# Optimization experiments

Measured on AMD Instinct MI355X. Metric: run time of the kernel, lower is better.

## Reference

```python
import jax, jax.numpy as jnp
import numpy as np

S = 10        # spiking_segment_count
TEMP = 50.0

def setup_inputs() -> dict:
    key = jax.random.key(0)
    ks = jax.random.split(key, 6)
    bs, din, dout = 2048, 1024, 1024
    x = jax.random.normal(ks[0], (bs, din), dtype=jnp.float32)
    t = jax.random.uniform(ks[1], (bs,), dtype=jnp.float32)  # in [0,1) subset of [-1,1]
    scale = 1.0 / np.sqrt(din)
    param_W = jax.random.normal(ks[2], (din, dout * S * 3), dtype=jnp.float32) * scale
    param_b = jax.random.normal(ks[3], (dout * S * 3,), dtype=jnp.float32) * 0.01
    norm_W = jax.random.normal(ks[4], (din, dout), dtype=jnp.float32) * scale
    norm_b = jax.random.normal(ks[5], (dout,), dtype=jnp.float32) * 0.01
    return {"x": x, "t": t, "param_W": param_W, "param_b": param_b,
            "norm_W": norm_W, "norm_b": norm_b}

def reference(x, t, param_W, param_b, norm_W, norm_b):
    bs = x.shape[0]
    dout = norm_W.shape[1]
    # param GEMM -> (bs, S, dout, 3)
    params = (x @ param_W + param_b).reshape(bs, S, dout, 3)
    weights = jax.nn.softmax(params[..., 0], axis=1)                 # (bs, S, dout)
    keypoints = jnp.concatenate(
        [jnp.zeros_like(weights[:, :1]), jnp.cumsum(weights, axis=1)], axis=1
    ) * 2.0 - 1.0                                                    # (bs, S+1, dout)
    slopes = jnp.tanh(params[..., 1])
    intercepts = params[..., 2]
    tt = t.reshape(-1, 1, 1)                                         # (bs, 1, 1)
    starts = keypoints[:, :S]
    ends = keypoints[:, 1:]
    residual = slopes * tt + intercepts                              # (bs, S, dout)
    validity = ((tt >= starts) & (tt < ends)) | ((tt == 1.0) & (ends == 1.0))
    vf = validity.astype(x.dtype)
    left_margin = jnp.sum((tt - starts) * vf, axis=1)                # (bs, dout)
    right_margin = jnp.sum((ends - tt) * vf, axis=1)
    lw = jax.nn.sigmoid(-TEMP * left_margin)
    rw = jax.nn.sigmoid(-TEMP * right_margin)
    lv = jnp.concatenate([vf[:, :1], vf[:, :-1]], axis=1)
    rv = jnp.concatenate([vf[:, 1:], vf[:, -1:]], axis=1)
    sw = -(lw + rw - 1.0)
    result = (lw * jnp.sum(residual * lv, axis=1)
              + sw * jnp.sum(residual * vf, axis=1)
              + rw * jnp.sum(residual * rv, axis=1))
    # norm == 'constant': subtract segment-wise integral, add norm_net(x)
    integral = jnp.sum(0.5 * slopes * (ends * ends - starts * starts)
                       + intercepts * weights, axis=1) * 0.5
    norm_target = x @ norm_W + norm_b
    return result - integral + norm_target
```

## Files before the change

kernel.cpp:

```cpp
#include <hip/hip_runtime.h>
#include <cstdint>
#include <cstddef>

#define BS    2048
#define DIN   1024
#define DOUT  1024
#define SSEG  10
#define NPAR  30720
#define NPK   20480
#define NCOL2 21504
#define NLG   10240
#define TAU   5e-5f
#define WL_CAP 1048576u

#define NB_SPLIT 2048
#define NB_NORM  1024
#define NB_TRW   2560

#define GEMM_BLKS 992

typedef _Float16 half_t;
typedef __attribute__((ext_vector_type(8))) _Float16 half8;
typedef __attribute__((ext_vector_type(4))) _Float16 half4;
typedef __attribute__((ext_vector_type(2))) _Float16 half2v;
typedef __attribute__((ext_vector_type(4))) float   floatx4;

__device__ __forceinline__ void gload16(const void* g, void* l) {
  __builtin_amdgcn_global_load_lds(
      (const __attribute__((address_space(1))) void*)g,
      (__attribute__((address_space(3))) void*)l, 16, 0, 0);
}

__global__ void k_zero(unsigned* c) { if (threadIdx.x == 0) *c = 0; }

__global__ __launch_bounds__(256) void k_prep(const float* __restrict__ x,
                                              half_t* __restrict__ xh,
                                              half_t* __restrict__ xl,
                                              const float* __restrict__ nW,
                                              const float* __restrict__ pW,
                                              half_t* __restrict__ wsm,
                                              half_t* __restrict__ wh,
                                              half_t* __restrict__ wlo,
                                              float* __restrict__ wlt,
                                              unsigned* __restrict__ cnt) {
  __shared__ float tile[32][384];
  int bid = blockIdx.x;
  int tid = threadIdx.x;

  if (bid < NB_SPLIT) {
    if (bid == 0 && tid == 0) *cnt = 0;
    int i = bid * 256 + tid;
    floatx4 v = ((const floatx4*)x)[i];
    half4 h, l;
    #pragma unroll
    for (int c = 0; c < 4; c++) { h[c] = (half_t)v[c]; l[c] = (half_t)(v[c] - (float)h[c]); }
    ((half4*)xh)[i] = h;
    ((half4*)xl)[i] = l;
    return;
  }

  if (bid < NB_SPLIT + NB_NORM) {
    int b2 = bid - NB_SPLIT;
    int col0 = (b2 & 31) * 32;
    int k0   = (b2 >> 5) * 32;
    int tx = tid & 31;
    int ty = tid >> 5;
    float* t33 = &tile[0][0];
    #pragma unroll
    for (int r = ty; r < 32; r += 8)
      t33[r * 33 + tx] = nW[(size_t)(k0 + r) * DOUT + col0 + tx];
    __syncthreads();
    #pragma unroll
    for (int r = ty; r < 32; r += 8)
      wsm[(size_t)(col0 + r + NPK) * DIN + k0 + tx] = (half_t)t33[tx * 33 + r];
    return;
  }

  int b3 = bid - NB_SPLIT - NB_NORM;
  int bx = b3 % 80;
  int k0 = (b3 / 80) * 32;
  int s  = bx >> 3;
  int d0 = (bx & 7) * 128;

  const float* sb = pW + (size_t)k0 * NPAR + bx * 384;
  for (int i = tid; i < 32 * 96; i += 256) {
    int r = i / 96, q = i - r * 96;
    ((floatx4*)&tile[r][0])[q] = ((const floatx4*)(sb + (size_t)r * NPAR))[q];
  }
  __syncthreads();

  for (int ci = tid; ci < 3072; ci += 256) {
    if (ci < 1024) {
      int rl = ci >> 2, kc = ci & 3;
      int jj = rl >> 1, cbit = rl & 1;
      int col = 3 * jj + 1 + cbit;
      half8 v;
      #pragma unroll
      for (int m = 0; m < 8; m++) v[m] = (half_t)tile[kc * 8 + m][col];
      *(half8*)(wsm + (size_t)(s * 2048 + 2 * (d0 + jj) + cbit) * DIN + k0 + kc * 8) = v;
    } else if (ci < 1536) {
      int u = ci - 1024;
      int jj = u >> 2, kc = u & 3;
      half8 v;
      #pragma unroll
      for (int m = 0; m < 8; m++) v[m] = (half_t)(tile[kc * 8 + m][3 * jj] * 32.0f);
      *(half8*)(wh + (size_t)(s * 1024 + d0 + jj) * DIN + k0 + kc * 8) = v;
    } else if (ci < 2048) {
      int u = ci - 1536;
      int jj = u >> 2, kc = u & 3;
      half8 v;
      #pragma unroll
      for (int m = 0; m < 8; m++) {
        float raw = tile[kc * 8 + m][3 * jj] * 32.0f;
        half_t h = (half_t)raw;
        v[m] = (half_t)(raw - (float)h);
      }
      *(half8*)(wlo + (size_t)(s * 1024 + d0 + jj) * DIN + k0 + kc * 8) = v;
    } else {
      int u = ci - 2048;
      int jj = u >> 3, kc = u & 7;
      floatx4 v;
      #pragma unroll
      for (int m = 0; m < 4; m++) v[m] = tile[kc * 4 + m][3 * jj];
      *(floatx4*)(wlt + (size_t)(s * 1024 + d0 + jj) * DIN + k0 + kc * 4) = v;
    }
  }
}

__global__ __launch_bounds__(512, 2) void k_gemm2(
    const half_t* __restrict__ xh, const half_t* __restrict__ xl,
    const half_t* __restrict__ wh, const half_t* __restrict__ wlo,
    const half_t* __restrict__ wsm,
    float* __restrict__ Lg, half_t* __restrict__ P,
    const float* __restrict__ pb, const float* __restrict__ nb) {
  __shared__ __attribute__((aligned(128))) char lds[131072];
  char* ldsA = lds;
  char* ldsB = lds + 65536;

  int bid = blockIdx.x;
  int tid = threadIdx.x;
  int w = tid >> 6, l = tid & 63;
  int wr = w >> 2, wc = w & 3;
  int l15 = l & 15, quad = l >> 4;

  int mode, mt, nt, KT;
  const half_t *A0, *A1, *A2, *B0, *B1, *B2;
  if (bid < 320) {
    int s = (bid & 7) * 40 + (bid >> 3);
    mode = 0; mt = s & 7; nt = s >> 3; KT = 96;
    A0 = xh; A1 = xl; A2 = xh; B0 = wh; B1 = wh; B2 = wlo;
  } else {
    int s2 = bid - 320;
    int s = (s2 & 7) * 84 + (s2 >> 3);
    mode = 1; mt = s & 7; nt = s >> 3; KT = 32;
    A0 = xh; A1 = xh; A2 = xh; B0 = wsm; B1 = wsm; B2 = wsm;
  }
  int m0 = mt * 256, n0 = nt * 256;

  int sp = (l & 7) ^ ((l >> 3) & 7);
  int srowA = m0 + w * 32 + 2 * (l >> 3) + (sp >> 2);
  int srowB = n0 + w * 32 + 2 * (l >> 3) + (sp >> 2);
  int scol = (sp & 3) * 8;

  int lofs = (l15 >> 1) * 128 + (((((l15 & 1) << 2) | quad) ^ (l15 >> 1)) << 4);
  const char* pA = ldsA + wr * 8192 + lofs;
  const char* pB = ldsB + wc * 4096 + lofs;

  auto stA = [&](int kt) {
    const half_t* As = (kt < 32) ? A0 : ((kt < 64) ? A1 : A2);
    const half_t* g = As + (size_t)srowA * DIN + (kt & 31) * 32 + scol;
    char* lb = ldsA + (kt & 3) * 16384 + w * 2048;
    gload16(g, lb);
    gload16(g + 16 * DIN, lb + 1024);
  };
  auto stB = [&](int kt) {
    const half_t* Bs = (kt < 32) ? B0 : ((kt < 64) ? B1 : B2);
    const half_t* g = Bs + (size_t)srowB * DIN + (kt & 31) * 32 + scol;
    char* lb = ldsB + (kt & 3) * 16384 + w * 2048;
    gload16(g, lb);
    gload16(g + 16 * DIN, lb + 1024);
  };

  floatx4 acc[8][4] = {};

  stA(0); stB(0); stA(1); stB(1); stA(2); stB(2);
  asm volatile("s_waitcnt vmcnt(8)" ::: "memory");
  __builtin_amdgcn_s_barrier();

  for (int kt = 0; kt < KT; ++kt) {
    const char* a = pA + (kt & 3) * 16384;
    const char* b = pB + (kt & 3) * 16384;
    half8 af[4], bf[4];
    #pragma unroll
    for (int ni = 0; ni < 4; ni++) bf[ni] = *(const half8*)(b + ni * 1024);
    #pragma unroll
    for (int mi = 0; mi < 4; mi++) af[mi] = *(const half8*)(a + mi * 1024);
    if (kt + 3 < KT) stA(kt + 3);
    __builtin_amdgcn_s_barrier();
    asm volatile("s_waitcnt lgkmcnt(0)" ::: "memory");
    __builtin_amdgcn_sched_barrier(0);
    __builtin_amdgcn_s_setprio(1);
    #pragma unroll
    for (int mi = 0; mi < 4; mi++)
      #pragma unroll
      for (int ni = 0; ni < 4; ni++)
        acc[mi][ni] = __builtin_amdgcn_mfma_f32_16x16x32_f16(af[mi], bf[ni], acc[mi][ni], 0, 0, 0);
    __builtin_amdgcn_s_setprio(0);
    __builtin_amdgcn_s_barrier();

    #pragma unroll
    for (int mi = 0; mi < 4; mi++) af[mi] = *(const half8*)(a + 4096 + mi * 1024);
    if (kt + 3 < KT) stB(kt + 3);
    __builtin_amdgcn_s_barrier();
    asm volatile("s_waitcnt lgkmcnt(0)" ::: "memory");
    __builtin_amdgcn_sched_barrier(0);
    __builtin_amdgcn_s_setprio(1);
    #pragma unroll
    for (int mi = 0; mi < 4; mi++)
      #pragma unroll
      for (int ni = 0; ni < 4; ni++)
        acc[4 + mi][ni] = __builtin_amdgcn_mfma_f32_16x16x32_f16(af[mi], bf[ni], acc[4 + mi][ni], 0, 0, 0);
    __builtin_amdgcn_s_setprio(0);
    if (kt < KT - 3)       { asm volatile("s_waitcnt vmcnt(8)" ::: "memory"); }
    else if (kt == KT - 3) { asm volatile("s_waitcnt vmcnt(4)" ::: "memory"); }
    else if (kt == KT - 2) { asm volatile("s_waitcnt vmcnt(0)" ::: "memory"); }
    __builtin_amdgcn_s_barrier();
  }

  int rbase = m0 + wr * 128 + quad * 4;
  int cbase = n0 + wc * 64 + l15;
  if (mode == 0) {
    #pragma unroll
    for (int ni = 0; ni < 4; ni++) {
      int col = cbase + ni * 16;
      float bias = pb[(col >> 10) * 3072 + (col & 1023) * 3];
      #pragma unroll
      for (int mi = 0; mi < 8; mi++) {
        int row = rbase + mi * 16;
        floatx4 v = acc[mi][ni];
        #pragma unroll
        for (int r = 0; r < 4; r++)
          Lg[(size_t)(row + r) * NLG + col] = v[r] * 0.03125f + bias;
      }
    }
  } else {
    #pragma unroll
    for (int ni = 0; ni < 4; ni++) {
      int col = cbase + ni * 16;
      float bias;
      if (col < NPK) {
        int s = col >> 11, rem = col & 2047;
        bias = pb[s * 3072 + 3 * (rem >> 1) + 1 + (rem & 1)];
      } else {
        bias = nb[col - NPK];
      }
      #pragma unroll
      for (int mi = 0; mi < 8; mi++) {
        int row = rbase + mi * 16;
        floatx4 v = acc[mi][ni];
        #pragma unroll
        for (int r = 0; r < 4; r++)
          P[(size_t)(row + r) * NCOL2 + col] = (half_t)(v[r] + bias);
      }
    }
  }
}

__device__ __forceinline__ float spiking_eval(const float* p, float tt, float* mind) {
  float mx = -1e30f;
  #pragma unroll
  for (int s = 0; s < SSEG; s++) mx = fmaxf(mx, p[3 * s]);
  float ew[10], wsum = 0.0f;
  #pragma unroll
  for (int s = 0; s < SSEG; s++) { ew[s] = __expf(p[3 * s] - mx); wsum += ew[s]; }
  float inv = 1.0f / wsum;

  float kp[11];
  kp[0] = -1.0f;
  float cum = 0.0f, md = 1e30f;
  #pragma unroll
  for (int s = 0; s < SSEG; s++) {
    cum += ew[s] * inv;
    kp[s + 1] = cum * 2.0f - 1.0f;
    md = fminf(md, fabsf(tt - kp[s + 1]));
  }
  *mind = md;

  float vf[10], resid[10];
  float lm = 0.0f, rm = 0.0f, integ = 0.0f;
  #pragma unroll
  for (int s = 0; s < SSEG; s++) {
    float p1 = p[3 * s + 1], p2 = p[3 * s + 2];
    float e2 = __expf(2.0f * fabsf(p1));
    float th = copysignf(1.0f - 2.0f / (e2 + 1.0f), p1);
    resid[s] = th * tt + p2;
    float st = kp[s], en = kp[s + 1];
    bool v = ((tt >= st) && (tt < en)) || ((tt == 1.0f) && (en == 1.0f));
    float vv = v ? 1.0f : 0.0f;
    vf[s] = vv;
    lm += (tt - st) * vv;
    rm += (en - tt) * vv;
    integ += 0.5f * th * (en * en - st * st) + p2 * (ew[s] * inv);
  }
  float resLV = 0.0f, resV = 0.0f, resRV = 0.0f;
  #pragma unroll
  for (int s = 0; s < SSEG; s++) {
    float lv = (s == 0) ? vf[0] : vf[s - 1];
    float rv = (s == 9) ? vf[9] : vf[s + 1];
    resLV += resid[s] * lv;
    resV  += resid[s] * vf[s];
    resRV += resid[s] * rv;
  }
  float lw = 1.0f / (1.0f + __expf(50.0f * lm));
  float rw = 1.0f / (1.0f + __expf(50.0f * rm));
  float swt = 1.0f - lw - rw;
  return lw * resLV + swt * resV + rw * resRV - 0.5f * integ + p[30];
}

__global__ __launch_bounds__(256) void k_pointwise(const half_t* __restrict__ P,
                                                   const float* __restrict__ Lg,
                                                   const float* __restrict__ t,
                                                   float* __restrict__ out,
                                                   unsigned* __restrict__ cnt,
                                                   unsigned* __restrict__ wl,
                                                   unsigned cap) {
  __shared__ __attribute__((aligned(16))) half_t sp[SSEG * 512];
  int b = blockIdx.x, dg = blockIdx.y, tid = threadIdx.x;
  const half_t* Pb = P + (size_t)b * NCOL2;
  for (int i = tid; i < SSEG * 64; i += 256) {
    int s = i >> 6, e = i & 63;
    ((uint4*)sp)[(s << 6) + e] = ((const uint4*)(Pb + s * 2048 + dg * 512))[e];
  }
  float tt = t[b];
  float nt = (float)Pb[NPK + dg * 256 + tid];
  const float* Lb = Lg + (size_t)b * NLG + dg * 256 + tid;
  __syncthreads();

  float p[31];
  #pragma unroll
  for (int s = 0; s < SSEG; s++) {
    p[3 * s] = Lb[s * 1024];
    half2v hv = ((const half2v*)sp)[s * 256 + tid];
    p[3 * s + 1] = (float)hv.x;
    p[3 * s + 2] = (float)hv.y;
  }
  p[30] = nt;
  float mind;
  float r = spiking_eval(p, tt, &mind);
  int d = dg * 256 + tid;
  out[(size_t)b * DOUT + d] = r;
  if (wl != nullptr && mind < TAU) {
    unsigned idx = atomicAdd(cnt, 1u);
    if (idx < cap) wl[idx] = ((unsigned)b << 10) | (unsigned)d;
  }
}

__global__ __launch_bounds__(256) void k_naive(const float* __restrict__ x,
                                               const float* __restrict__ t,
                                               const float* __restrict__ pW,
                                               const float* __restrict__ pb,
                                               const float* __restrict__ nW,
                                               const float* __restrict__ nb,
                                               float* __restrict__ out,
                                               unsigned* __restrict__ cnt,
                                               unsigned* __restrict__ wl,
                                               unsigned cap) {
  __shared__ float xs[DIN];
  int b = blockIdx.x, dg = blockIdx.y, tid = threadIdx.x;
  for (int i = tid; i < DIN; i += 256) xs[i] = x[(size_t)b * DIN + i];
  __syncthreads();
  int d = dg * 256 + tid;
  float acc[31];
  #pragma unroll
  for (int i = 0; i < 31; i++) acc[i] = 0.0f;
  for (int k = 0; k < DIN; k++) {
    float xv = xs[k];
    const float* wr = pW + (size_t)k * NPAR + 3 * d;
    #pragma unroll
    for (int s = 0; s < SSEG; s++) {
      acc[3 * s]     += xv * wr[s * 3072];
      acc[3 * s + 1] += xv * wr[s * 3072 + 1];
      acc[3 * s + 2] += xv * wr[s * 3072 + 2];
    }
    acc[30] += xv * nW[(size_t)k * DOUT + d];
  }
  #pragma unroll
  for (int s = 0; s < SSEG; s++) {
    acc[3 * s]     += pb[s * 3072 + 3 * d];
    acc[3 * s + 1] += pb[s * 3072 + 3 * d + 1];
    acc[3 * s + 2] += pb[s * 3072 + 3 * d + 2];
  }
  acc[30] += nb[d];
  float mind;
  float r = spiking_eval(acc, t[b], &mind);
  out[(size_t)b * DOUT + d] = r;
  if (wl != nullptr && mind < TAU) {
    unsigned idx = atomicAdd(cnt, 1u);
    if (idx < cap) wl[idx] = ((unsigned)b << 10) | (unsigned)d;
  }
}

__global__ __launch_bounds__(256) void k_redo(const float* __restrict__ x,
                                              const float* __restrict__ t,
                                              const float* __restrict__ pW,
                                              const float* __restrict__ pb,
                                              const float* __restrict__ nW,
                                              const float* __restrict__ nb,
                                              const half_t* __restrict__ P,
                                              const float* __restrict__ WLt,
                                              int haveP,
                                              const unsigned* __restrict__ cnt,
                                              const unsigned* __restrict__ wl,
                                              unsigned cap,
                                              float* __restrict__ out) {
  unsigned n = *cnt;
  if (n > cap) n = cap;
  int lane = threadIdx.x & 63;
  unsigned wave = (blockIdx.x * 256 + threadIdx.x) >> 6;
  unsigned nwaves = (gridDim.x * 256) >> 6;

  for (unsigned e = wave; e < n; e += nwaves) {
    unsigned code = wl[e];
    int b = (int)(code >> 10), d = (int)(code & 1023);

    double lg[10], sl[10], ic[10], nt = 0.0;
    #pragma unroll
    for (int s = 0; s < SSEG; s++) { lg[s] = 0.0; sl[s] = 0.0; ic[s] = 0.0; }

    if (haveP) {
      for (int k = lane; k < DIN; k += 64) {
        double xv = (double)x[(size_t)b * DIN + k];
        #pragma unroll
        for (int s = 0; s < SSEG; s++)
          lg[s] += xv * (double)WLt[(size_t)(s * 1024 + d) * DIN + k];
      }
    } else {
      for (int k = lane; k < DIN; k += 64) {
        double xv = (double)x[(size_t)b * DIN + k];
        const float* wr = pW + (size_t)k * NPAR + 3 * d;
        #pragma unroll
        for (int s = 0; s < SSEG; s++) {
          lg[s] += xv * (double)wr[s * 3072];
          sl[s] += xv * (double)wr[s * 3072 + 1];
          ic[s] += xv * (double)wr[s * 3072 + 2];
        }
        nt += xv * (double)nW[(size_t)k * DOUT + d];
      }
    }
    #pragma unroll
    for (int off = 32; off > 0; off >>= 1) {
      #pragma unroll
      for (int s = 0; s < SSEG; s++) lg[s] += __shfl_down(lg[s], off);
      if (!haveP) {
        #pragma unroll
        for (int s = 0; s < SSEG; s++) {
          sl[s] += __shfl_down(sl[s], off);
          ic[s] += __shfl_down(ic[s], off);
        }
        nt += __shfl_down(nt, off);
      }
    }

    if (lane == 0) {
      double slope[10], icpt[10], ntv;
      if (haveP) {
        const half_t* Pr = P + (size_t)b * NCOL2;
        #pragma unroll
        for (int s = 0; s < SSEG; s++) {
          slope[s] = tanh((double)(float)Pr[s * 2048 + 2 * d]);
          icpt[s]  = (double)(float)Pr[s * 2048 + 2 * d + 1];
        }
        ntv = (double)(float)Pr[NPK + d];
      } else {
        #pragma unroll
        for (int s = 0; s < SSEG; s++) {
          slope[s] = tanh(sl[s] + (double)pb[s * 3072 + 3 * d + 1]);
          icpt[s]  = ic[s] + (double)pb[s * 3072 + 3 * d + 2];
        }
        ntv = nt + (double)nb[d];
      }
      #pragma unroll
      for (int s = 0; s < SSEG; s++) lg[s] += (double)pb[s * 3072 + 3 * d];

      double mx = -1e300;
      #pragma unroll
      for (int s = 0; s < SSEG; s++) mx = fmax(mx, lg[s]);
      double ew[10], ws = 0.0;
      #pragma unroll
      for (int s = 0; s < SSEG; s++) { ew[s] = exp(lg[s] - mx); ws += ew[s]; }

      double kp[11];
      kp[0] = -1.0;
      double cum = 0.0;
      #pragma unroll
      for (int s = 0; s < SSEG; s++) { cum += ew[s] / ws; kp[s + 1] = cum * 2.0 - 1.0; }

      double tt = (double)t[b];
      double vf[10], resid[10], lm = 0.0, rm = 0.0, integ = 0.0;
      #pragma unroll
      for (int s = 0; s < SSEG; s++) {
        double st = kp[s], en = kp[s + 1];
        bool v = ((tt >= st) && (tt < en)) || ((tt == 1.0) && (en == 1.0));
        double vv = v ? 1.0 : 0.0;
        vf[s] = vv;
        resid[s] = slope[s] * tt + icpt[s];
        lm += (tt - st) * vv;
        rm += (en - tt) * vv;
        integ += 0.5 * slope[s] * (en * en - st * st) + icpt[s] * (ew[s] / ws);
      }
      double rLV = 0.0, rV = 0.0, rRV = 0.0;
      #pragma unroll
      for (int s = 0; s < SSEG; s++) {
        double lv = (s == 0) ? vf[0] : vf[s - 1];
        double rv = (s == 9) ? vf[9] : vf[s + 1];
        rLV += resid[s] * lv;
        rV  += resid[s] * vf[s];
        rRV += resid[s] * rv;
      }
      double lw = 1.0 / (1.0 + exp(50.0 * lm));
      double rw = 1.0 / (1.0 + exp(50.0 * rm));
      double res = lw * rLV + (1.0 - lw - rw) * rV + rw * rRV - 0.5 * integ + ntv;
      out[(size_t)b * DOUT + d] = (float)res;
    }
  }
}

extern "C" void kernel_launch(void* const* d_in, const int* in_sizes, int n_in,
                              void* d_out, int out_size, void* d_ws, size_t ws_size,
                              hipStream_t stream) {
  const float* x  = (const float*)d_in[0];
  const float* t  = (const float*)d_in[1];
  const float* pW = (const float*)d_in[2];
  const float* pb = (const float*)d_in[3];
  const float* nW = (const float*)d_in[4];
  const float* nb = (const float*)d_in[5];
  float* out = (float*)d_out;

  const size_t o_cnt = 0;
  const size_t o_wl  = 64;
  const size_t o_xh  = o_wl  + (size_t)WL_CAP * 4;
  const size_t o_xl  = o_xh  + (size_t)BS * DIN * 2;
  const size_t o_wsm = o_xl  + (size_t)BS * DIN * 2;
  const size_t o_wh  = o_wsm + (size_t)NCOL2 * DIN * 2;
  const size_t o_wlo = o_wh  + (size_t)NLG * DIN * 2;
  const size_t o_wlt = o_wlo + (size_t)NLG * DIN * 2;
  const size_t o_p   = o_wlt + (size_t)NLG * DIN * 4;
  const size_t o_lg  = o_p   + (size_t)BS * NCOL2 * 2;
  const size_t need  = o_lg  + (size_t)BS * NLG * 4;

  bool have_wl = ws_size >= 1024 * 1024;
  unsigned* cnt = (unsigned*)((char*)d_ws + o_cnt);
  unsigned* wl  = (unsigned*)((char*)d_ws + o_wl);
  unsigned cap  = 0;
  if (have_wl) {
    size_t avail = (ws_size >= need) ? (size_t)WL_CAP
                                     : (ws_size - o_wl) / 4;
    cap = (unsigned)(avail < WL_CAP ? avail : WL_CAP);
  }

  if (ws_size >= need) {
    half_t* xh  = (half_t*)((char*)d_ws + o_xh);
    half_t* xl  = (half_t*)((char*)d_ws + o_xl);
    half_t* wsm = (half_t*)((char*)d_ws + o_wsm);
    half_t* wh  = (half_t*)((char*)d_ws + o_wh);
    half_t* wlo = (half_t*)((char*)d_ws + o_wlo);
    float*  wlt = (float*)((char*)d_ws + o_wlt);
    half_t* P   = (half_t*)((char*)d_ws + o_p);
    float*  Lg  = (float*)((char*)d_ws + o_lg);

    k_prep<<<NB_SPLIT + NB_NORM + NB_TRW, 256, 0, stream>>>(x, xh, xl, nW, pW,
                                                            wsm, wh, wlo, wlt, cnt);
    k_gemm2<<<GEMM_BLKS, 512, 0, stream>>>(xh, xl, wh, wlo, wsm, Lg, P, pb, nb);
    k_pointwise<<<dim3(BS, DOUT / 256), 256, 0, stream>>>(P, Lg, t, out, cnt,
                                                          have_wl ? wl : nullptr, cap);
    if (have_wl)
      k_redo<<<256, 256, 0, stream>>>(x, t, pW, pb, nW, nb, P, wlt, 1, cnt, wl, cap, out);
  } else {
    if (have_wl) k_zero<<<1, 64, 0, stream>>>(cnt);
    k_naive<<<dim3(BS, DOUT / 256), 256, 0, stream>>>(x, t, pW, pb, nW, nb, out, cnt,
                                                      have_wl ? wl : nullptr, cap);
    if (have_wl)
      k_redo<<<256, 256, 0, stream>>>(x, t, pW, pb, nW, nb, nullptr, nullptr, 0,
                                      cnt, wl, cap, out);
  }
}
```

Baseline: 561.2 us.

## Drop fp32 transposed logit weights, merge A/B staging, simplify block mapping and pointwise loads

Removes the fp32 transposed logit-weight copy written by the prep kernel, so the redo kernel now recomputes all params from the original pW and nW layout. The GEMM interleaves A and B tiles in one LDS stage per k-step and issues both loads together. It also drops the XCD-aware block swizzle in favour of a linear mapping. The pointwise kernel reads P straight from global memory instead of staging it through LDS. This saves prep writes and bandwidth, but redo work per flagged element grows and the simpler block mapping may hurt L2 locality.

```diff
diff --git a/kernel.cpp b/kernel.cpp
--- a/kernel.cpp
+++ b/kernel.cpp
@@ -41,7 +41,6 @@
                                               half_t* __restrict__ wsm,
                                               half_t* __restrict__ wh,
                                               half_t* __restrict__ wlo,
-                                              float* __restrict__ wlt,
                                               unsigned* __restrict__ cnt) {
   __shared__ float tile[32][384];
   int bid = blockIdx.x;
@@ -89,7 +88,7 @@
   }
   __syncthreads();
 
-  for (int ci = tid; ci < 3072; ci += 256) {
+  for (int ci = tid; ci < 2048; ci += 256) {
     if (ci < 1024) {
       int rl = ci >> 2, kc = ci & 3;
       int jj = rl >> 1, cbit = rl & 1;
@@ -105,7 +104,7 @@
       #pragma unroll
       for (int m = 0; m < 8; m++) v[m] = (half_t)(tile[kc * 8 + m][3 * jj] * 32.0f);
       *(half8*)(wh + (size_t)(s * 1024 + d0 + jj) * DIN + k0 + kc * 8) = v;
-    } else if (ci < 2048) {
+    } else {
       int u = ci - 1536;
       int jj = u >> 2, kc = u & 3;
       half8 v;
@@ -116,13 +115,6 @@
         v[m] = (half_t)(raw - (float)h);
       }
       *(half8*)(wlo + (size_t)(s * 1024 + d0 + jj) * DIN + k0 + kc * 8) = v;
-    } else {
-      int u = ci - 2048;
-      int jj = u >> 3, kc = u & 7;
-      floatx4 v;
-      #pragma unroll
-      for (int m = 0; m < 4; m++) v[m] = tile[kc * 4 + m][3 * jj];
-      *(floatx4*)(wlt + (size_t)(s * 1024 + d0 + jj) * DIN + k0 + kc * 4) = v;
     }
   }
 }
@@ -134,8 +126,6 @@
     float* __restrict__ Lg, half_t* __restrict__ P,
     const float* __restrict__ pb, const float* __restrict__ nb) {
   __shared__ __attribute__((aligned(128))) char lds[131072];
-  char* ldsA = lds;
-  char* ldsB = lds + 65536;
 
   int bid = blockIdx.x;
   int tid = threadIdx.x;
@@ -144,17 +134,8 @@
   int l15 = l & 15, quad = l >> 4;
 
   int mode, mt, nt, KT;
-  const half_t *A0, *A1, *A2, *B0, *B1, *B2;
-  if (bid < 320) {
-    int s = (bid & 7) * 40 + (bid >> 3);
-    mode = 0; mt = s & 7; nt = s >> 3; KT = 96;
-    A0 = xh; A1 = xl; A2 = xh; B0 = wh; B1 = wh; B2 = wlo;
-  } else {
-    int s2 = bid - 320;
-    int s = (s2 & 7) * 84 + (s2 >> 3);
-    mode = 1; mt = s & 7; nt = s >> 3; KT = 32;
-    A0 = xh; A1 = xh; A2 = xh; B0 = wsm; B1 = wsm; B2 = wsm;
-  }
+  if (bid < 320) { mode = 0; mt = bid & 7; nt = bid >> 3; KT = 96; }
+  else { int s2 = bid - 320; mode = 1; mt = s2 & 7; nt = s2 >> 3; KT = 32; }
   int m0 = mt * 256, n0 = nt * 256;
 
   int sp = (l & 7) ^ ((l >> 3) & 7);
@@ -163,39 +144,37 @@
   int scol = (sp & 3) * 8;
 
   int lofs = (l15 >> 1) * 128 + (((((l15 & 1) << 2) | quad) ^ (l15 >> 1)) << 4);
-  const char* pA = ldsA + wr * 8192 + lofs;
-  const char* pB = ldsB + wc * 4096 + lofs;
-
-  auto stA = [&](int kt) {
-    const half_t* As = (kt < 32) ? A0 : ((kt < 64) ? A1 : A2);
-    const half_t* g = As + (size_t)srowA * DIN + (kt & 31) * 32 + scol;
-    char* lb = ldsA + (kt & 3) * 16384 + w * 2048;
-    gload16(g, lb);
-    gload16(g + 16 * DIN, lb + 1024);
+
+  const half_t* gA0 = xh + (size_t)srowA * DIN + scol;
+  const half_t* gA1 = (mode == 0 ? xl : xh) + (size_t)srowA * DIN + scol;
+  const half_t* gB01 = (mode == 0 ? wh : wsm) + (size_t)srowB * DIN + scol;
+  const half_t* gB2 = (mode == 0 ? wlo : wsm) + (size_t)srowB * DIN + scol;
+
+  auto stage = [&](int kt) {
+    char* base = lds + ((kt & 3) * 32768) + w * 2048;
+    const half_t* ga = (kt < 32 ? gA0 : (kt < 64 ? gA1 : gA0)) + (kt & 31) * 32;
+    const half_t* gb = (kt < 64 ? gB01 : gB2) + (kt & 31) * 32;
+    gload16(ga, base);            gload16(ga + 16 * DIN, base + 1024);
+    gload16(gb, base + 16384);    gload16(gb + 16 * DIN, base + 16384 + 1024);
   };
-  auto stB = [&](int kt) {
-    const half_t* Bs = (kt < 32) ? B0 : ((kt < 64) ? B1 : B2);
-    const half_t* g = Bs + (size_t)srowB * DIN + (kt & 31) * 32 + scol;
-    char* lb = ldsB + (kt & 3) * 16384 + w * 2048;
-    gload16(g, lb);
-    gload16(g + 16 * DIN, lb + 1024);
-  };
 
   floatx4 acc[8][4] = {};
 
-  stA(0); stB(0); stA(1); stB(1); stA(2); stB(2);
+  stage(0); stage(1); stage(2);
   asm volatile("s_waitcnt vmcnt(8)" ::: "memory");
   __builtin_amdgcn_s_barrier();
 
   for (int kt = 0; kt < KT; ++kt) {
-    const char* a = pA + (kt & 3) * 16384;
-    const char* b = pB + (kt & 3) * 16384;
-    half8 af[4], bf[4];
+    const char* base = lds + (kt & 3) * 32768;
+    const char* a = base + wr * 8192 + lofs;
+    const char* b = base + 16384 + wc * 4096 + lofs;
+
+    half8 bf[4], af[4];
     #pragma unroll
     for (int ni = 0; ni < 4; ni++) bf[ni] = *(const half8*)(b + ni * 1024);
     #pragma unroll
     for (int mi = 0; mi < 4; mi++) af[mi] = *(const half8*)(a + mi * 1024);
-    if (kt + 3 < KT) stA(kt + 3);
+    if (kt + 3 < KT) stage(kt + 3);
     __builtin_amdgcn_s_barrier();
     asm volatile("s_waitcnt lgkmcnt(0)" ::: "memory");
     __builtin_amdgcn_sched_barrier(0);
@@ -208,9 +187,9 @@
     __builtin_amdgcn_s_setprio(0);
     __builtin_amdgcn_s_barrier();
 
-    #pragma unroll
-    for (int mi = 0; mi < 4; mi++) af[mi] = *(const half8*)(a + 4096 + mi * 1024);
-    if (kt + 3 < KT) stB(kt + 3);
+    half8 ag[4];
+    #pragma unroll
+    for (int mi = 0; mi < 4; mi++) ag[mi] = *(const half8*)(a + 4096 + mi * 1024);
     __builtin_amdgcn_s_barrier();
     asm volatile("s_waitcnt lgkmcnt(0)" ::: "memory");
     __builtin_amdgcn_sched_barrier(0);
@@ -219,12 +198,21 @@
     for (int mi = 0; mi < 4; mi++)
       #pragma unroll
       for (int ni = 0; ni < 4; ni++)
-        acc[4 + mi][ni] = __builtin_amdgcn_mfma_f32_16x16x32_f16(af[mi], bf[ni], acc[4 + mi][ni], 0, 0, 0);
+        acc[4 + mi][ni] = __builtin_amdgcn_mfma_f32_16x16x32_f16(ag[mi], bf[ni], acc[4 + mi][ni], 0, 0, 0);
     __builtin_amdgcn_s_setprio(0);
-    if (kt < KT - 3)       { asm volatile("s_waitcnt vmcnt(8)" ::: "memory"); }
-    else if (kt == KT - 3) { asm volatile("s_waitcnt vmcnt(4)" ::: "memory"); }
-    else if (kt == KT - 2) { asm volatile("s_waitcnt vmcnt(0)" ::: "memory"); }
-    __builtin_amdgcn_s_barrier();
+    if (kt < KT - 3) {
+      __builtin_amdgcn_sched_barrier(0);
+      asm volatile("s_waitcnt vmcnt(8)" ::: "memory");
+      __builtin_amdgcn_s_barrier();
+    } else if (kt == KT - 3) {
+      __builtin_amdgcn_sched_barrier(0);
+      asm volatile("s_waitcnt vmcnt(4)" ::: "memory");
+      __builtin_amdgcn_s_barrier();
+    } else if (kt == KT - 2) {
+      __builtin_amdgcn_sched_barrier(0);
+      asm volatile("s_waitcnt vmcnt(0)" ::: "memory");
+      __builtin_amdgcn_s_barrier();
+    }
   }
 
   int rbase = m0 + wr * 128 + quad * 4;
@@ -324,30 +312,23 @@
                                                    unsigned* __restrict__ cnt,
                                                    unsigned* __restrict__ wl,
                                                    unsigned cap) {
-  __shared__ __attribute__((aligned(16))) half_t sp[SSEG * 512];
   int b = blockIdx.x, dg = blockIdx.y, tid = threadIdx.x;
+  int d = dg * 256 + tid;
   const half_t* Pb = P + (size_t)b * NCOL2;
-  for (int i = tid; i < SSEG * 64; i += 256) {
-    int s = i >> 6, e = i & 63;
-    ((uint4*)sp)[(s << 6) + e] = ((const uint4*)(Pb + s * 2048 + dg * 512))[e];
-  }
+  const float* Lb = Lg + (size_t)b * NLG + d;
   float tt = t[b];
-  float nt = (float)Pb[NPK + dg * 256 + tid];
-  const float* Lb = Lg + (size_t)b * NLG + dg * 256 + tid;
-  __syncthreads();
 
   float p[31];
   #pragma unroll
   for (int s = 0; s < SSEG; s++) {
     p[3 * s] = Lb[s * 1024];
-    half2v hv = ((const half2v*)sp)[s * 256 + tid];
+    half2v hv = *(const half2v*)(Pb + s * 2048 + 2 * d);
     p[3 * s + 1] = (float)hv.x;
     p[3 * s + 2] = (float)hv.y;
   }
-  p[30] = nt;
+  p[30] = (float)Pb[NPK + d];
   float mind;
   float r = spiking_eval(p, tt, &mind);
-  int d = dg * 256 + tid;
   out[(size_t)b * DOUT + d] = r;
   if (wl != nullptr && mind < TAU) {
     unsigned idx = atomicAdd(cnt, 1u);
@@ -406,9 +387,6 @@
                                               const float* __restrict__ pb,
                                               const float* __restrict__ nW,
                                               const float* __restrict__ nb,
-                                              const half_t* __restrict__ P,
-                                              const float* __restrict__ WLt,
-                                              int haveP,
                                               const unsigned* __restrict__ cnt,
                                               const unsigned* __restrict__ wl,
                                               unsigned cap,
@@ -427,58 +405,36 @@
     #pragma unroll
     for (int s = 0; s < SSEG; s++) { lg[s] = 0.0; sl[s] = 0.0; ic[s] = 0.0; }
 
-    if (haveP) {
-      for (int k = lane; k < DIN; k += 64) {
-        double xv = (double)x[(size_t)b * DIN + k];
-        #pragma unroll
-        for (int s = 0; s < SSEG; s++)
-          lg[s] += xv * (double)WLt[(size_t)(s * 1024 + d) * DIN + k];
-      }
-    } else {
-      for (int k = lane; k < DIN; k += 64) {
-        double xv = (double)x[(size_t)b * DIN + k];
-        const float* wr = pW + (size_t)k * NPAR + 3 * d;
-        #pragma unroll
-        for (int s = 0; s < SSEG; s++) {
-          lg[s] += xv * (double)wr[s * 3072];
-          sl[s] += xv * (double)wr[s * 3072 + 1];
-          ic[s] += xv * (double)wr[s * 3072 + 2];
-        }
-        nt += xv * (double)nW[(size_t)k * DOUT + d];
-      }
+    for (int k = lane; k < DIN; k += 64) {
+      double xv = (double)x[(size_t)b * DIN + k];
+      const float* wr = pW + (size_t)k * NPAR + 3 * d;
+      #pragma unroll
+      for (int s = 0; s < SSEG; s++) {
+        lg[s] += xv * (double)wr[s * 3072];
+        sl[s] += xv * (double)wr[s * 3072 + 1];
+        ic[s] += xv * (double)wr[s * 3072 + 2];
+      }
+      nt += xv * (double)nW[(size_t)k * DOUT + d];
     }
     #pragma unroll
     for (int off = 32; off > 0; off >>= 1) {
       #pragma unroll
-      for (int s = 0; s < SSEG; s++) lg[s] += __shfl_down(lg[s], off);
-      if (!haveP) {
-        #pragma unroll
-        for (int s = 0; s < SSEG; s++) {
-          sl[s] += __shfl_down(sl[s], off);
-          ic[s] += __shfl_down(ic[s], off);
-        }
-        nt += __shfl_down(nt, off);
-      }
+      for (int s = 0; s < SSEG; s++) {
+        lg[s] += __shfl_down(lg[s], off);
+        sl[s] += __shfl_down(sl[s], off);
+        ic[s] += __shfl_down(ic[s], off);
+      }
+      nt += __shfl_down(nt, off);
     }
 
     if (lane == 0) {
       double slope[10], icpt[10], ntv;
-      if (haveP) {
-        const half_t* Pr = P + (size_t)b * NCOL2;
-        #pragma unroll
-        for (int s = 0; s < SSEG; s++) {
-          slope[s] = tanh((double)(float)Pr[s * 2048 + 2 * d]);
-          icpt[s]  = (double)(float)Pr[s * 2048 + 2 * d + 1];
-        }
-        ntv = (double)(float)Pr[NPK + d];
-      } else {
-        #pragma unroll
-        for (int s = 0; s < SSEG; s++) {
-          slope[s] = tanh(sl[s] + (double)pb[s * 3072 + 3 * d + 1]);
-          icpt[s]  = ic[s] + (double)pb[s * 3072 + 3 * d + 2];
-        }
-        ntv = nt + (double)nb[d];
-      }
+      #pragma unroll
+      for (int s = 0; s < SSEG; s++) {
+        slope[s] = tanh(sl[s] + (double)pb[s * 3072 + 3 * d + 1]);
+        icpt[s]  = ic[s] + (double)pb[s * 3072 + 3 * d + 2];
+      }
+      ntv = nt + (double)nb[d];
       #pragma unroll
       for (int s = 0; s < SSEG; s++) lg[s] += (double)pb[s * 3072 + 3 * d];
 
@@ -543,8 +499,7 @@
   const size_t o_wsm = o_xl  + (size_t)BS * DIN * 2;
   const size_t o_wh  = o_wsm + (size_t)NCOL2 * DIN * 2;
   const size_t o_wlo = o_wh  + (size_t)NLG * DIN * 2;
-  const size_t o_wlt = o_wlo + (size_t)NLG * DIN * 2;
-  const size_t o_p   = o_wlt + (size_t)NLG * DIN * 4;
+  const size_t o_p   = o_wlo + (size_t)NLG * DIN * 2;
   const size_t o_lg  = o_p   + (size_t)BS * NCOL2 * 2;
   const size_t need  = o_lg  + (size_t)BS * NLG * 4;
 
@@ -564,23 +519,21 @@
     half_t* wsm = (half_t*)((char*)d_ws + o_wsm);
     half_t* wh  = (half_t*)((char*)d_ws + o_wh);
     half_t* wlo = (half_t*)((char*)d_ws + o_wlo);
-    float*  wlt = (float*)((char*)d_ws + o_wlt);
     half_t* P   = (half_t*)((char*)d_ws + o_p);
     float*  Lg  = (float*)((char*)d_ws + o_lg);
 
     k_prep<<<NB_SPLIT + NB_NORM + NB_TRW, 256, 0, stream>>>(x, xh, xl, nW, pW,
-                                                            wsm, wh, wlo, wlt, cnt);
+                                                            wsm, wh, wlo, cnt);
     k_gemm2<<<GEMM_BLKS, 512, 0, stream>>>(xh, xl, wh, wlo, wsm, Lg, P, pb, nb);
     k_pointwise<<<dim3(BS, DOUT / 256), 256, 0, stream>>>(P, Lg, t, out, cnt,
                                                           have_wl ? wl : nullptr, cap);
     if (have_wl)
-      k_redo<<<256, 256, 0, stream>>>(x, t, pW, pb, nW, nb, P, wlt, 1, cnt, wl, cap, out);
+      k_redo<<<256, 256, 0, stream>>>(x, t, pW, pb, nW, nb, cnt, wl, cap, out);
   } else {
     if (have_wl) k_zero<<<1, 64, 0, stream>>>(cnt);
     k_naive<<<dim3(BS, DOUT / 256), 256, 0, stream>>>(x, t, pW, pb, nW, nb, out, cnt,
                                                       have_wl ? wl : nullptr, cap);
     if (have_wl)
-      k_redo<<<256, 256, 0, stream>>>(x, t, pW, pb, nW, nb, nullptr, nullptr, 0,
-                                      cnt, wl, cap, out);
-  }
-}
+      k_redo<<<256, 256, 0, stream>>>(x, t, pW, pb, nW, nb, cnt, wl, cap, out);
+  }
+}
```

Result: slower. 756.1 us (+34.7%).
